# Kernel tuning notes

Measured on AMD Instinct MI355X. Metric: run time of the kernel, lower is better.

## Reference

```python
import jax, jax.numpy as jnp
import numpy as np

D = 256      # input_dim
H = 8        # n_heads
HD = D // H  # head_dim = 32
B = 8
S = 127      # seq_len (feature tokens)
N = S + 1    # new_seq (CLS + features)
LN_EPS = 1e-5


def setup_inputs() -> dict:
    key = jax.random.key(0)
    ks = jax.random.split(key, 20)
    g = 0.02
    inp = {
        "desc_embeddings": jax.random.normal(ks[0], (B, S, D), jnp.float32),
        "name_value_embeddings": jax.random.normal(ks[1], (B, N, D), jnp.float32),
        # q/k/v projections (stored [in, out])
        "wq": jax.random.normal(ks[2], (D, D), jnp.float32) * g,
        "bq": jnp.zeros((D,), jnp.float32),
        "wk": jax.random.normal(ks[3], (D, D), jnp.float32) * g,
        "bk": jnp.zeros((D,), jnp.float32),
        "wv": jax.random.normal(ks[4], (D, D), jnp.float32) * g,
        "bv": jnp.zeros((D,), jnp.float32),
        # edge_update: Linear(2D->D), LayerNorm(D), ReLU, Linear(D->D)
        "ew1": jax.random.normal(ks[5], (2 * D, D), jnp.float32) * g,
        "eb1": jnp.zeros((D,), jnp.float32),
        "ln_g": jnp.ones((D,), jnp.float32),
        "ln_b": jnp.zeros((D,), jnp.float32),
        "ew2": jax.random.normal(ks[6], (D, D), jnp.float32) * g,
        "eb2": jnp.zeros((D,), jnp.float32),
        # attn_proj: Linear(3*head_dim -> 1)
        "attn_w": jax.random.normal(ks[7], (3 * HD,), jnp.float32) * g,
        "attn_b": jnp.zeros((), jnp.float32),
        # out_proj
        "wo": jax.random.normal(ks[8], (D, D), jnp.float32) * g,
        "bo": jnp.zeros((D,), jnp.float32),
    }
    return inp


def _forward(desc, nv, wq, bq, wk, bk, wv, bv, ew1, eb1, ln_g, ln_b, ew2, eb2,
             attn_w, attn_b, wo, bo):
    b, n, d = nv.shape
    s = n - 1
    # new adjacency: [1:,1:] = ones minus diag; row 0 (CLS->var) = 1; col 0 = 0; [0,0]=0
    adj = jnp.zeros((n, n), nv.dtype)
    adj = adj.at[1:, 1:].set(1.0 - jnp.eye(s, dtype=nv.dtype))
    adj = adj.at[0, 1:].set(1.0)
    adj = jnp.broadcast_to(adj, (b, n, n))  # [B,N,N]

    # edge attributes: var-var pairs concat(desc_i, desc_j); CLS row/col concat(desc_j, desc_j)
    var_edge = jnp.concatenate([
        jnp.broadcast_to(desc[:, :, None, :], (b, s, s, d)),
        jnp.broadcast_to(desc[:, None, :, :], (b, s, s, d)),
    ], axis=-1)                                   # [B,S,S,2D]
    cls_edge = jnp.concatenate([desc, desc], -1)  # [B,S,2D]
    ea = jnp.zeros((b, n, n, 2 * d), nv.dtype)
    ea = ea.at[:, 1:, 1:, :].set(var_edge)
    ea = ea.at[:, 0, 1:, :].set(cls_edge)
    ea = ea.at[:, 1:, 0, :].set(cls_edge)

    # edge MLP: Linear -> LayerNorm -> ReLU -> Linear
    h = ea @ ew1 + eb1                            # [B,N,N,D]
    mu = jnp.mean(h, -1, keepdims=True)
    var = jnp.mean((h - mu) ** 2, -1, keepdims=True)
    h = (h - mu) * jax.lax.rsqrt(var + LN_EPS) * ln_g + ln_b
    h = jax.nn.relu(h)
    e = h @ ew2 + eb2                             # [B,N,N,D]
    e = e.reshape(b, n, n, H, HD).transpose(0, 3, 1, 2, 4)  # [B,H,N,N,hd]
    e = e * adj[:, None, :, :, None]

    def heads(x, w, bias):
        return (x @ w + bias).reshape(b, n, H, HD).transpose(0, 2, 1, 3)  # [B,H,N,hd]

    q = heads(nv, wq, bq)
    k = heads(nv, wk, bk)
    v = heads(nv, wv, bv)

    # attn_proj(cat(q_i, k_j, e_ij)) decomposes additively over the three chunks
    w_q, w_k, w_e = attn_w[:HD], attn_w[HD:2 * HD], attn_w[2 * HD:]
    aq = jnp.einsum('bhid,d->bhi', q, w_q)
    ak = jnp.einsum('bhjd,d->bhj', k, w_k)
    ae = jnp.einsum('bhijd,d->bhij', e, w_e)
    scores = aq[:, :, :, None] + ak[:, :, None, :] + ae + attn_b  # [B,H,N,N]
    scores = scores + (adj[:, None] == 0).astype(scores.dtype) * (-1e9)
    attn = jax.nn.softmax(scores, axis=-1)

    ctx = jnp.einsum('bhij,bhjd->bhid', attn, v)                  # [B,H,N,hd]
    ctx = ctx.transpose(0, 2, 1, 3).reshape(b, n, d)
    out = ctx @ wo + bo
    return out, attn


def reference(desc_embeddings, name_value_embeddings, wq, bq, wk, bk, wv, bv,
              ew1, eb1, ln_g, ln_b, ew2, eb2, attn_w, attn_b, wo, bo):
    return _forward(desc_embeddings, name_value_embeddings, wq, bq, wk, bk, wv, bv,
                    ew1, eb1, ln_g, ln_b, ew2, eb2, attn_w, attn_b, wo, bo)
```

## Files before the change

kernel.cpp:

```cpp
#include <hip/hip_runtime.h>
#include <math.h>

namespace {
constexpr int D = 256;
constexpr int H = 8;
constexpr int HD = 32;
constexpr int B = 8;
constexpr int S = 127;
constexpr int N = 128;
constexpr float LN_EPS = 1e-5f;

constexpr int WS_P1T = 0;
constexpr int WS_P2T = WS_P1T + B * D * N;
constexpr int WS_V   = WS_P2T + B * D * N;
constexpr int WS_AQ  = WS_V + B * N * D;
constexpr int WS_AK  = WS_AQ + B * H * N;
constexpr int WS_FQK = WS_AK + B * H * N;
constexpr int WS_V2  = WS_FQK + D * 16;
constexpr int WS_BF  = WS_V2 + D * H;
constexpr int WS_ST  = WS_BF + 32;
constexpr int WS_RSTD = WS_ST + B * 512;
constexpr int WS_MB   = WS_RSTD + B * N * N;

typedef float f32x2 __attribute__((ext_vector_type(2)));
union F4 { float4 v; f32x2 h[2]; float f[4]; };
}

__global__ __launch_bounds__(256) void k1_fold(
    const float* __restrict__ wq, const float* __restrict__ wk,
    const float* __restrict__ ew2, const float* __restrict__ bq,
    const float* __restrict__ bk, const float* __restrict__ eb2,
    const float* __restrict__ attn_w, float* __restrict__ ws) {
  float* FQK = ws + WS_FQK;
  float* V2T = ws + WS_V2;
  float* BF  = ws + WS_BF;
  const int tg = blockIdx.x * 256 + threadIdx.x;
  if (tg < 6144) {
    const int mat = tg >> 11;
    const int rem = tg & 2047;
    const int c = rem >> 3;
    const int h = rem & 7;
    const float* W = (mat == 0) ? wq : (mat == 1) ? wk : ew2;
    const float* aw = attn_w + mat * HD;
    const float* wrow = W + c * D + h * HD;
    float s = 0.f;
#pragma unroll
    for (int d = 0; d < HD; ++d) s = fmaf(wrow[d], aw[d], s);
    if (mat < 2) FQK[c * 16 + mat * 8 + h] = s;
    else         V2T[h * D + c] = s;
  } else if (tg < 6168) {
    const int idx = tg - 6144;
    const int mat = idx >> 3;
    const int h = idx & 7;
    const float* bias = (mat == 0) ? bq : (mat == 1) ? bk : eb2;
    const float* aw = attn_w + mat * HD;
    float s = 0.f;
#pragma unroll
    for (int d = 0; d < HD; ++d) s = fmaf(bias[h * HD + d], aw[d], s);
    BF[mat * 8 + h] = s;
  }
}

__global__ __launch_bounds__(256) void kA_pre(
    const float* __restrict__ desc, const float* __restrict__ ew1,
    const float* __restrict__ eb1,
    const float* __restrict__ nv, const float* __restrict__ wv,
    const float* __restrict__ bv, float* __restrict__ ws) {
  const int blk = blockIdx.x;
  const int t = threadIdx.x;
  __shared__ float rows[4][264];
  __shared__ float aqred[4][64];
  __shared__ float statred[4][16];

  if (blk < 256) {
    float* P1Tf = ws + WS_P1T;
    float* P2Tf = ws + WS_P2T;
    const int b = blk >> 5;
    const int i0 = (blk & 31) * 4;
    for (int k = t; k < 4 * D; k += 256) {
      const int r = k >> 8, c = k & (D - 1);
      const int row = i0 + r;
      rows[r][c] = (row < S) ? desc[(b * S + row) * D + c] : 0.f;
    }
    __syncthreads();
    float a1[4], a2[4];
#pragma unroll
    for (int ii = 0; ii < 4; ++ii) { a1[ii] = 0.f; a2[ii] = 0.f; }
    for (int c2 = 0; c2 < D; c2 += 4) {
      float w1[4], w2[4];
#pragma unroll
      for (int e = 0; e < 4; ++e) {
        w1[e] = ew1[(c2 + e) * D + t];
        w2[e] = ew1[(D + c2 + e) * D + t];
      }
#pragma unroll
      for (int ii = 0; ii < 4; ++ii) {
        F4 dv; dv.v = *(const float4*)&rows[ii][c2];
#pragma unroll
        for (int e = 0; e < 4; ++e) {
          a1[ii] = fmaf(dv.f[e], w1[e], a1[ii]);
          a2[ii] = fmaf(dv.f[e], w2[e], a2[ii]);
        }
      }
    }
    const float ebv = eb1[t];
    const int pbase = (b * 64 + (t >> 2)) * 512 + (t & 3);
#pragma unroll
    for (int ii = 0; ii < 4; ++ii) {
      if (i0 + ii < S) {
        P1Tf[pbase + (i0 + ii) * 4] = a1[ii] + ebv;
        P2Tf[pbase + (i0 + ii) * 4] = a2[ii];
      }
    }
    float stv[16];
#pragma unroll
    for (int ii = 0; ii < 4; ++ii) {
      const float v1 = a1[ii] + ebv;
      const float v2x = a2[ii];
      stv[ii * 4 + 0] = v1;
      stv[ii * 4 + 1] = v1 * v1;
      stv[ii * 4 + 2] = v2x;
      stv[ii * 4 + 3] = v2x * v2x;
    }
#pragma unroll
    for (int st = 0; st < 16; ++st) {
#pragma unroll
      for (int o = 1; o < 64; o <<= 1) stv[st] += __shfl_xor(stv[st], o);
    }
    const int w = t >> 6;
    if ((t & 63) == 0) {
#pragma unroll
      for (int st = 0; st < 16; ++st) statred[w][st] = stv[st];
    }
    __syncthreads();
    if (t < 16) {
      const int ii = t >> 2, st = t & 3;
      if (i0 + ii < S) {
        const float s = statred[0][t] + statred[1][t]
                      + statred[2][t] + statred[3][t];
        ws[WS_ST + b * 512 + st * 128 + (i0 + ii)] = s;
      }
    }
  } else {
    float* Vf  = ws + WS_V;
    float* AQ  = ws + WS_AQ;
    float* AK  = ws + WS_AK;
    const float* FQK = ws + WS_FQK;
    const float* BF  = ws + WS_BF;
    const int blk2 = blk - 256;
    const int b = blk2 >> 5;
    const int j0 = (blk2 & 31) * 4;
    for (int k = t; k < 4 * D; k += 256) {
      const int r = k >> 8, c = k & (D - 1);
      rows[r][c] = nv[(b * N + j0 + r) * D + c];
    }
    __syncthreads();
    float acc[4];
#pragma unroll
    for (int jj = 0; jj < 4; ++jj) acc[jj] = 0.f;
    for (int c2 = 0; c2 < D; c2 += 4) {
      float wvv[4];
#pragma unroll
      for (int e = 0; e < 4; ++e) wvv[e] = wv[(c2 + e) * D + t];
#pragma unroll
      for (int jj = 0; jj < 4; ++jj) {
        F4 x; x.v = *(const float4*)&rows[jj][c2];
#pragma unroll
        for (int e = 0; e < 4; ++e) acc[jj] = fmaf(x.f[e], wvv[e], acc[jj]);
      }
    }
    const float bias = bv[t];
#pragma unroll
    for (int jj = 0; jj < 4; ++jj)
      Vf[(b * N + j0 + jj) * D + t] = acc[jj] + bias;

    const int pair = t & 63;
    const int cq = t >> 6;
    const int il = pair >> 4, oi = pair & 15;
    float s = 0.f;
    for (int c = cq * 64; c < cq * 64 + 64; ++c)
      s = fmaf(rows[il][c], FQK[c * 16 + oi], s);
    aqred[cq][pair] = s;
    __syncthreads();
    if (t < 64) {
      const int il2 = t >> 4, oi2 = t & 15;
      float s2 = aqred[0][t] + aqred[1][t] + aqred[2][t] + aqred[3][t] + BF[oi2];
      if (oi2 < 8) AQ[(b * H + oi2) * N + j0 + il2] = s2;
      else         AK[(b * H + (oi2 - 8)) * N + j0 + il2] = s2;
    }
  }
}

__global__ __launch_bounds__(512) void kG_stats(float* __restrict__ ws) {
  const int bid = blockIdx.x;
  const int wg = (bid & 7) * 32 + (bid >> 3);
  const int b = wg >> 5;
  const int ip0 = (wg & 31) * 4;
  const int t = threadIdx.x;
  const int jp = t & 127;
  const int cg = t >> 7;

  __shared__ float p1t[1024];
  __shared__ float gred[4][4][128];

  const float* P1Tf = ws + WS_P1T;
  const float4* P24 = reinterpret_cast<const float4*>(ws + WS_P2T);
  const float* ST = ws + WS_ST + b * 512;
  float* RST = ws + WS_RSTD + b * N * N;
  float* MBP = ws + WS_MB + b * N * N;
  const int base4 = b * 64 * 128;

  for (int k = t; k < 1024; k += 512) {
    const int r = k >> 8, c = k & 255;
    const int row = ip0 + r;
    p1t[r * 256 + c] = (row < S)
        ? P1Tf[(b * 64 + (c >> 2)) * 512 + row * 4 + (c & 3)] : 0.f;
  }
  F4 pp[16];
#pragma unroll
  for (int cc = 0; cc < 16; ++cc)
    pp[cc].v = P24[base4 + (cg * 16 + cc) * 128 + jp];
  __syncthreads();

  float g[4] = {0.f, 0.f, 0.f, 0.f};
#pragma unroll
  for (int cc = 0; cc < 16; ++cc) {
    const int c4 = cg * 16 + cc;
#pragma unroll
    for (int r = 0; r < 4; ++r) {
      F4 p1; p1.v = *(const float4*)&p1t[r * 256 + c4 * 4];
      g[r] = fmaf(pp[cc].f[0], p1.f[0], g[r]);
      g[r] = fmaf(pp[cc].f[1], p1.f[1], g[r]);
      g[r] = fmaf(pp[cc].f[2], p1.f[2], g[r]);
      g[r] = fmaf(pp[cc].f[3], p1.f[3], g[r]);
    }
  }
#pragma unroll
  for (int r = 0; r < 4; ++r) gred[cg][r][jp] = g[r];
  __syncthreads();
  {
    const int r2 = t >> 7, jp2 = t & 127;
    const float G = gred[0][r2][jp2] + gred[1][r2][jp2]
                  + gred[2][r2][jp2] + gred[3][r2][jp2];
    const int ip = ip0 + r2;
    const float S1 = ST[0 * 128 + ip], Q1 = ST[1 * 128 + ip];
    const float S2 = ST[2 * 128 + jp2], Q2 = ST[3 * 128 + jp2];
    const float mean = (S1 + S2) * (1.f / 256.f);
    const float var = (Q1 + Q2 + 2.f * G) * (1.f / 256.f) - mean * mean;
    const float rstd = 1.f / sqrtf(var + LN_EPS);
    RST[ip * N + jp2] = rstd;
    MBP[ip * N + jp2] = -mean * rstd;
  }
}

__global__ __launch_bounds__(512) void k4_attn(
    const float* __restrict__ ws,
    const float* __restrict__ ln_g, const float* __restrict__ ln_b,
    const float* __restrict__ attn_bp, float* __restrict__ attnp) {
  const int bid = blockIdx.x;
  const int wg = (bid & 7) * 64 + (bid >> 3);
  const int b = wg >> 6;
  const int i0 = (wg & 63) * 2;
  const int t = threadIdx.x;
  const int jl = t & 127;
  const int cq = t >> 7;

  __shared__ float v2s[H * D];
  __shared__ float gbs[2 * D];
  __shared__ float p1e[2][D];
  __shared__ float dsh[4][128][9];
  __shared__ float aqs[2][8];
  __shared__ float redm[8][2], reds[8][2];

  const float* P1Tf = ws + WS_P1T;
  const float* AQ   = ws + WS_AQ;
  const float* AK   = ws + WS_AK;
  const float* BF   = ws + WS_BF;
  const float* v2p  = ws + WS_V2;
  const float* RST  = ws + WS_RSTD + b * N * N;
  const float* MBP  = ws + WS_MB + b * N * N;

  reinterpret_cast<float4*>(v2s)[t] = reinterpret_cast<const float4*>(v2p)[t];
  if (t < 256) { gbs[t] = ln_g[t]; gbs[256 + t] = ln_b[t]; }
  {
    const int r = t >> 8, c = t & 255;
    const int row = i0 + r - 1;
    p1e[r][c] = (row >= 0)
        ? P1Tf[(b * 64 + (c >> 2)) * 512 + row * 4 + (c & 3)] : 0.f;
  }
  if (t < 16) {
    const int r = t >> 3, h = t & 7;
    aqs[r][h] = AQ[(b * H + h) * N + i0 + r] + BF[16 + h] + attn_bp[0];
  }

  const int jm1 = (jl == 0) ? 0 : jl - 1;
  const bool blk0 = (i0 == 0);
  f32x2 rstd2[2], mb2[2];
#pragma unroll
  for (int r = 0; r < 2; ++r) {
    const int irow = i0 + r;
    const int ip = (irow == 0) ? jm1 : (irow - 1);
    const float rs = RST[ip * N + jm1];
    const float mb = MBP[ip * N + jm1];
    rstd2[r].x = rs; rstd2[r].y = rs;
    mb2[r].x = mb; mb2[r].y = mb;
  }
  float akr[2];
#pragma unroll
  for (int hh = 0; hh < 2; ++hh)
    akr[hh] = AK[(b * H + cq * 2 + hh) * N + jl];
  const f32x2 zero2 = {0.f, 0.f};
  __syncthreads();

  const float4* P14 = reinterpret_cast<const float4*>(ws + WS_P1T);
  const float4* P24 = reinterpret_cast<const float4*>(ws + WS_P2T);
  const int base4 = b * 64 * 128;
  const int c4lo = cq * 16;

  f32x2 dt2[2][8];
#pragma unroll
  for (int r = 0; r < 2; ++r)
#pragma unroll
    for (int h = 0; h < 8; ++h) dt2[r][h] = zero2;
  F4 p2c;
  p2c.v = P24[base4 + c4lo * 128 + jm1];
  for (int cc = 0; cc < 16; ++cc) {
    const int c4 = c4lo + cc;
    F4 p2 = p2c;
    if (cc < 15) p2c.v = P24[base4 + (c4 + 1) * 128 + jm1];
    F4 g4; g4.v = *(const float4*)&gbs[c4 * 4];
    F4 b4; b4.v = *(const float4*)&gbs[256 + c4 * 4];
    F4 p1r[2];
    if (blk0) p1r[0].v = P14[base4 + c4 * 128 + jm1];
    else      p1r[0].v = *(const float4*)&p1e[0][c4 * 4];
    p1r[1].v = *(const float4*)&p1e[1][c4 * 4];
    f32x2 w2[2][2];
#pragma unroll
    for (int r = 0; r < 2; ++r) {
#pragma unroll
      for (int pp = 0; pp < 2; ++pp) {
        const f32x2 u2 = p1r[r].h[pp] + p2.h[pp];
        const f32x2 zt2 = __builtin_elementwise_fma(u2, rstd2[r], mb2[r]);
        const f32x2 z2 = __builtin_elementwise_fma(zt2, g4.h[pp], b4.h[pp]);
        w2[r][pp] = __builtin_elementwise_max(z2, zero2);
      }
    }
#pragma unroll
    for (int h = 0; h < 8; ++h) {
      F4 v2v; v2v.v = *(const float4*)&v2s[h * D + c4 * 4];
      dt2[0][h] = __builtin_elementwise_fma(w2[0][0], v2v.h[0], dt2[0][h]);
      dt2[0][h] = __builtin_elementwise_fma(w2[0][1], v2v.h[1], dt2[0][h]);
      dt2[1][h] = __builtin_elementwise_fma(w2[1][0], v2v.h[0], dt2[1][h]);
      dt2[1][h] = __builtin_elementwise_fma(w2[1][1], v2v.h[1], dt2[1][h]);
    }
  }

  const int w = t >> 6;
  for (int r = 0; r < 2; ++r) {
#pragma unroll
    for (int h = 0; h < 8; ++h) dsh[cq][jl][h] = dt2[r][h].x + dt2[r][h].y;
    __syncthreads();
    const int irow = i0 + r;
    const bool masked = (jl == 0) || (jl == irow);
    float sc[2], pr[2];
#pragma unroll
    for (int hh = 0; hh < 2; ++hh) {
      const int h = cq * 2 + hh;
      const float dsum = dsh[0][jl][h] + dsh[1][jl][h]
                       + dsh[2][jl][h] + dsh[3][jl][h];
      const float v = aqs[r][h] + akr[hh] + dsum;
      sc[hh] = masked ? -INFINITY : v;
    }
    float mx[2];
#pragma unroll
    for (int hh = 0; hh < 2; ++hh) {
      float v = sc[hh];
#pragma unroll
      for (int o = 1; o < 64; o <<= 1) v = fmaxf(v, __shfl_xor(v, o));
      mx[hh] = v;
    }
    if ((t & 63) == 0) { redm[w][0] = mx[0]; redm[w][1] = mx[1]; }
    __syncthreads();
#pragma unroll
    for (int hh = 0; hh < 2; ++hh) {
      const float m = fmaxf(redm[w][hh], redm[w ^ 1][hh]);
      pr[hh] = expf(sc[hh] - m);
    }
    float sm[2];
#pragma unroll
    for (int hh = 0; hh < 2; ++hh) {
      float v = pr[hh];
#pragma unroll
      for (int o = 1; o < 64; o <<= 1) v += __shfl_xor(v, o);
      sm[hh] = v;
    }
    if ((t & 63) == 0) { reds[w][0] = sm[0]; reds[w][1] = sm[1]; }
    __syncthreads();
#pragma unroll
    for (int hh = 0; hh < 2; ++hh) {
      const int h = cq * 2 + hh;
      const float at = pr[hh] / (reds[w][hh] + reds[w ^ 1][hh]);
      attnp[((b * H + h) * N + irow) * N + jl] = at;
    }
    __syncthreads();
  }
}

__global__ __launch_bounds__(1024) void k5_out(
    const float* __restrict__ ws, const float* __restrict__ attnp,
    const float* __restrict__ wo, const float* __restrict__ bo,
    float* __restrict__ outp) {
  const int bid = blockIdx.x;
  const int wg = (bid & 7) * 32 + (bid >> 3);
  const int b = wg >> 5;
  const int i0 = (wg & 31) * 4;
  const int t = threadIdx.x;
  const int r = t >> 8, c = t & 255;

  __shared__ float attn_sh[4][H][N];
  __shared__ float ctxs[4][260];

  for (int k = t; k < 4 * H * N; k += 1024) {
    const int rr = k >> 10, h = (k >> 7) & 7, j = k & 127;
    attn_sh[rr][h][j] = attnp[((b * H + h) * N + i0 + rr) * N + j];
  }
  __syncthreads();

  const int hh = c >> 5;
  const float* Vb = ws + WS_V + b * N * D + c;
  float acc = 0.f;
  for (int j = 0; j < N; ++j)
    acc = fmaf(attn_sh[r][hh][j], Vb[j * D], acc);
  ctxs[r][c] = acc;
  __syncthreads();

  float o = bo[c];
  for (int c2 = 0; c2 < D; c2 += 4) {
    F4 cx; cx.v = *(const float4*)&ctxs[r][c2];
    o = fmaf(cx.f[0], wo[(c2 + 0) * D + c], o);
    o = fmaf(cx.f[1], wo[(c2 + 1) * D + c], o);
    o = fmaf(cx.f[2], wo[(c2 + 2) * D + c], o);
    o = fmaf(cx.f[3], wo[(c2 + 3) * D + c], o);
  }
  outp[(b * N + i0 + r) * D + c] = o;
}

extern "C" void kernel_launch(void* const* d_in, const int* in_sizes, int n_in,
                              void* d_out, int out_size, void* d_ws, size_t ws_size,
                              hipStream_t stream) {
  (void)in_sizes; (void)n_in; (void)out_size; (void)ws_size;
  const float* desc = (const float*)d_in[0];
  const float* nv   = (const float*)d_in[1];
  const float* wq   = (const float*)d_in[2];
  const float* bq   = (const float*)d_in[3];
  const float* wk   = (const float*)d_in[4];
  const float* bk   = (const float*)d_in[5];
  const float* wv   = (const float*)d_in[6];
  const float* bv   = (const float*)d_in[7];
  const float* ew1  = (const float*)d_in[8];
  const float* eb1  = (const float*)d_in[9];
  const float* ln_g = (const float*)d_in[10];
  const float* ln_b = (const float*)d_in[11];
  const float* ew2  = (const float*)d_in[12];
  const float* eb2  = (const float*)d_in[13];
  const float* aw   = (const float*)d_in[14];
  const float* ab   = (const float*)d_in[15];
  const float* wo   = (const float*)d_in[16];
  const float* bo   = (const float*)d_in[17];

  float* ws   = (float*)d_ws;
  float* outp = (float*)d_out;
  float* attnp = outp + B * N * D;

  k1_fold<<<25, 256, 0, stream>>>(wq, wk, ew2, bq, bk, eb2, aw, ws);
  kA_pre<<<512, 256, 0, stream>>>(desc, ew1, eb1, nv, wv, bv, ws);
  kG_stats<<<256, 512, 0, stream>>>(ws);
  k4_attn<<<B * 64, 512, 0, stream>>>(ws, ln_g, ln_b, ab, attnp);
  k5_out<<<256, 1024, 0, stream>>>(ws, attnp, wo, bo, outp);
}
```

Measured before the change: 56.75 us.

## Restructure pre and output kernels with float4 register tiling and split-K reductions

The P1/P2 projection, the V projection and the output kernel now use float4 weight loads with per-thread register tiles over output columns and rows. The output kernel drops from 1024 to 512 threads and splits the j and K dimensions across thread groups, adding a shared-memory reduction step. The FQK matrix is staged in shared memory for the aq/ak dot products, and the per-row stats reduction is simplified. This is meant to cut redundant scalar global weight loads and improve memory coalescing. The cost is extra shared memory, more synchronization, and an idle-thread imbalance in the V path, where only 64 threads do the GEMM.

```diff
diff --git a/kernel.cpp b/kernel.cpp
--- a/kernel.cpp
+++ b/kernel.cpp
@@ -69,77 +69,73 @@
   const int blk = blockIdx.x;
   const int t = threadIdx.x;
   __shared__ float rows[4][264];
-  __shared__ float aqred[4][64];
-  __shared__ float statred[4][16];
+  __shared__ float fqks[D * 16];
+  __shared__ float aqred2[2][64];
 
   if (blk < 256) {
     float* P1Tf = ws + WS_P1T;
     float* P2Tf = ws + WS_P2T;
     const int b = blk >> 5;
     const int i0 = (blk & 31) * 4;
-    for (int k = t; k < 4 * D; k += 256) {
-      const int r = k >> 8, c = k & (D - 1);
+    {
+      const int r = t >> 6, c4 = t & 63;
       const int row = i0 + r;
-      rows[r][c] = (row < S) ? desc[(b * S + row) * D + c] : 0.f;
-    }
-    __syncthreads();
-    float a1[4], a2[4];
-#pragma unroll
-    for (int ii = 0; ii < 4; ++ii) { a1[ii] = 0.f; a2[ii] = 0.f; }
-    for (int c2 = 0; c2 < D; c2 += 4) {
-      float w1[4], w2[4];
+      F4 dv;
+      if (row < S) dv.v = *(const float4*)&desc[(b * S + row) * D + c4 * 4];
+      else         dv.v = make_float4(0.f, 0.f, 0.f, 0.f);
+      *(float4*)&rows[r][c4 * 4] = dv.v;
+    }
+    __syncthreads();
+    const int o4 = t & 63;
+    const int grp = t >> 6;
+    const int m = grp >> 1;
+    const int rp = grp & 1;
+    const float* W = ew1 + m * D * D;
+    F4 a0, a1;
+    a0.v = make_float4(0.f, 0.f, 0.f, 0.f);
+    a1.v = make_float4(0.f, 0.f, 0.f, 0.f);
+    for (int c2 = 0; c2 < D; ++c2) {
+      F4 w; w.v = *(const float4*)&W[c2 * D + o4 * 4];
+      const float s0 = rows[rp * 2][c2];
+      const float s1 = rows[rp * 2 + 1][c2];
 #pragma unroll
       for (int e = 0; e < 4; ++e) {
-        w1[e] = ew1[(c2 + e) * D + t];
-        w2[e] = ew1[(D + c2 + e) * D + t];
+        a0.f[e] = fmaf(s0, w.f[e], a0.f[e]);
+        a1.f[e] = fmaf(s1, w.f[e], a1.f[e]);
       }
-#pragma unroll
-      for (int ii = 0; ii < 4; ++ii) {
-        F4 dv; dv.v = *(const float4*)&rows[ii][c2];
-#pragma unroll
-        for (int e = 0; e < 4; ++e) {
-          a1[ii] = fmaf(dv.f[e], w1[e], a1[ii]);
-          a2[ii] = fmaf(dv.f[e], w2[e], a2[ii]);
-        }
-      }
-    }
-    const float ebv = eb1[t];
-    const int pbase = (b * 64 + (t >> 2)) * 512 + (t & 3);
-#pragma unroll
-    for (int ii = 0; ii < 4; ++ii) {
-      if (i0 + ii < S) {
-        P1Tf[pbase + (i0 + ii) * 4] = a1[ii] + ebv;
-        P2Tf[pbase + (i0 + ii) * 4] = a2[ii];
-      }
-    }
-    float stv[16];
-#pragma unroll
-    for (int ii = 0; ii < 4; ++ii) {
-      const float v1 = a1[ii] + ebv;
-      const float v2x = a2[ii];
-      stv[ii * 4 + 0] = v1;
-      stv[ii * 4 + 1] = v1 * v1;
-      stv[ii * 4 + 2] = v2x;
-      stv[ii * 4 + 3] = v2x * v2x;
-    }
-#pragma unroll
-    for (int st = 0; st < 16; ++st) {
-#pragma unroll
-      for (int o = 1; o < 64; o <<= 1) stv[st] += __shfl_xor(stv[st], o);
-    }
-    const int w = t >> 6;
-    if ((t & 63) == 0) {
-#pragma unroll
-      for (int st = 0; st < 16; ++st) statred[w][st] = stv[st];
-    }
-    __syncthreads();
-    if (t < 16) {
-      const int ii = t >> 2, st = t & 3;
-      if (i0 + ii < S) {
-        const float s = statred[0][t] + statred[1][t]
-                      + statred[2][t] + statred[3][t];
-        ws[WS_ST + b * 512 + st * 128 + (i0 + ii)] = s;
-      }
+    }
+    F4 ebv;
+    if (m == 0) ebv.v = *(const float4*)&eb1[o4 * 4];
+    else        ebv.v = make_float4(0.f, 0.f, 0.f, 0.f);
+    F4 o0, o1;
+#pragma unroll
+    for (int e = 0; e < 4; ++e) {
+      o0.f[e] = a0.f[e] + ebv.f[e];
+      o1.f[e] = a1.f[e] + ebv.f[e];
+    }
+    float* PT = (m == 0) ? P1Tf : P2Tf;
+    const int rbase = (b * 64 + o4) * 512;
+    const int row0i = i0 + rp * 2;
+    const int row1i = row0i + 1;
+    if (row0i < S) *(float4*)&PT[rbase + row0i * 4] = o0.v;
+    if (row1i < S) *(float4*)&PT[rbase + row1i * 4] = o1.v;
+    float sv0 = 0.f, qv0 = 0.f, sv1 = 0.f, qv1 = 0.f;
+#pragma unroll
+    for (int e = 0; e < 4; ++e) {
+      sv0 += o0.f[e]; qv0 = fmaf(o0.f[e], o0.f[e], qv0);
+      sv1 += o1.f[e]; qv1 = fmaf(o1.f[e], o1.f[e], qv1);
+    }
+#pragma unroll
+    for (int o = 1; o < 64; o <<= 1) {
+      sv0 += __shfl_xor(sv0, o);
+      qv0 += __shfl_xor(qv0, o);
+      sv1 += __shfl_xor(sv1, o);
+      qv1 += __shfl_xor(qv1, o);
+    }
+    if (o4 == 0) {
+      float* STW = ws + WS_ST + b * 512 + m * 256;
+      if (row0i < S) { STW[row0i] = sv0; STW[128 + row0i] = qv0; }
+      if (row1i < S) { STW[row1i] = sv1; STW[128 + row1i] = qv1; }
     }
   } else {
     float* Vf  = ws + WS_V;
@@ -150,43 +146,54 @@
     const int blk2 = blk - 256;
     const int b = blk2 >> 5;
     const int j0 = (blk2 & 31) * 4;
-    for (int k = t; k < 4 * D; k += 256) {
-      const int r = k >> 8, c = k & (D - 1);
-      rows[r][c] = nv[(b * N + j0 + r) * D + c];
-    }
-    __syncthreads();
-    float acc[4];
-#pragma unroll
-    for (int jj = 0; jj < 4; ++jj) acc[jj] = 0.f;
-    for (int c2 = 0; c2 < D; c2 += 4) {
-      float wvv[4];
-#pragma unroll
-      for (int e = 0; e < 4; ++e) wvv[e] = wv[(c2 + e) * D + t];
-#pragma unroll
-      for (int jj = 0; jj < 4; ++jj) {
-        F4 x; x.v = *(const float4*)&rows[jj][c2];
-#pragma unroll
-        for (int e = 0; e < 4; ++e) acc[jj] = fmaf(x.f[e], wvv[e], acc[jj]);
+    {
+      const int r = t >> 6, c4 = t & 63;
+      *(float4*)&rows[r][c4 * 4] =
+          *(const float4*)&nv[(b * N + j0 + r) * D + c4 * 4];
+      float4* fq4 = (float4*)fqks;
+      const float4* FQK4 = (const float4*)FQK;
+#pragma unroll
+      for (int k = 0; k < 4; ++k) fq4[k * 256 + t] = FQK4[k * 256 + t];
+    }
+    __syncthreads();
+    if (t < 64) {
+      const int o4 = t;
+      F4 acc[4];
+#pragma unroll
+      for (int r = 0; r < 4; ++r) acc[r].v = make_float4(0.f, 0.f, 0.f, 0.f);
+      for (int c2 = 0; c2 < D; ++c2) {
+        F4 w; w.v = *(const float4*)&wv[c2 * D + o4 * 4];
+#pragma unroll
+        for (int r = 0; r < 4; ++r) {
+          const float s = rows[r][c2];
+#pragma unroll
+          for (int e = 0; e < 4; ++e)
+            acc[r].f[e] = fmaf(s, w.f[e], acc[r].f[e]);
+        }
       }
-    }
-    const float bias = bv[t];
-#pragma unroll
-    for (int jj = 0; jj < 4; ++jj)
-      Vf[(b * N + j0 + jj) * D + t] = acc[jj] + bias;
-
-    const int pair = t & 63;
-    const int cq = t >> 6;
-    const int il = pair >> 4, oi = pair & 15;
-    float s = 0.f;
-    for (int c = cq * 64; c < cq * 64 + 64; ++c)
-      s = fmaf(rows[il][c], FQK[c * 16 + oi], s);
-    aqred[cq][pair] = s;
+      F4 b4; b4.v = *(const float4*)&bv[o4 * 4];
+#pragma unroll
+      for (int r = 0; r < 4; ++r) {
+#pragma unroll
+        for (int e = 0; e < 4; ++e) acc[r].f[e] += b4.f[e];
+        *(float4*)&Vf[(b * N + j0 + r) * D + o4 * 4] = acc[r].v;
+      }
+    } else if (t < 192) {
+      const int idx = t - 64;
+      const int il = idx >> 5;
+      const int oi = idx & 15;
+      const int ch = (idx >> 4) & 1;
+      float s = 0.f;
+      for (int c = ch * 128; c < ch * 128 + 128; ++c)
+        s = fmaf(rows[il][c], fqks[c * 16 + oi], s);
+      aqred2[ch][il * 16 + oi] = s;
+    }
     __syncthreads();
     if (t < 64) {
-      const int il2 = t >> 4, oi2 = t & 15;
-      float s2 = aqred[0][t] + aqred[1][t] + aqred[2][t] + aqred[3][t] + BF[oi2];
-      if (oi2 < 8) AQ[(b * H + oi2) * N + j0 + il2] = s2;
-      else         AK[(b * H + (oi2 - 8)) * N + j0 + il2] = s2;
+      const int il = t >> 4, oi = t & 15;
+      const float s2 = aqred2[0][t] + aqred2[1][t] + BF[oi];
+      if (oi < 8) AQ[(b * H + oi) * N + j0 + il] = s2;
+      else        AK[(b * H + (oi - 8)) * N + j0 + il] = s2;
     }
   }
 }
@@ -406,7 +413,7 @@
   }
 }
 
-__global__ __launch_bounds__(1024) void k5_out(
+__global__ __launch_bounds__(512) void k5_out(
     const float* __restrict__ ws, const float* __restrict__ attnp,
     const float* __restrict__ wo, const float* __restrict__ bo,
     float* __restrict__ outp) {
@@ -415,34 +422,82 @@
   const int b = wg >> 5;
   const int i0 = (wg & 31) * 4;
   const int t = threadIdx.x;
-  const int r = t >> 8, c = t & 255;
-
-  __shared__ float attn_sh[4][H][N];
+  const int o4 = t & 63;
+  const int grp = t >> 6;
+
+  __shared__ float attn_sh[4][H][136];
+  __shared__ float red[4][8][64][4];
   __shared__ float ctxs[4][260];
 
-  for (int k = t; k < 4 * H * N; k += 1024) {
-    const int rr = k >> 10, h = (k >> 7) & 7, j = k & 127;
-    attn_sh[rr][h][j] = attnp[((b * H + h) * N + i0 + rr) * N + j];
-  }
-  __syncthreads();
-
-  const int hh = c >> 5;
-  const float* Vb = ws + WS_V + b * N * D + c;
-  float acc = 0.f;
-  for (int j = 0; j < N; ++j)
-    acc = fmaf(attn_sh[r][hh][j], Vb[j * D], acc);
-  ctxs[r][c] = acc;
-  __syncthreads();
-
-  float o = bo[c];
-  for (int c2 = 0; c2 < D; c2 += 4) {
-    F4 cx; cx.v = *(const float4*)&ctxs[r][c2];
-    o = fmaf(cx.f[0], wo[(c2 + 0) * D + c], o);
-    o = fmaf(cx.f[1], wo[(c2 + 1) * D + c], o);
-    o = fmaf(cx.f[2], wo[(c2 + 2) * D + c], o);
-    o = fmaf(cx.f[3], wo[(c2 + 3) * D + c], o);
-  }
-  outp[(b * N + i0 + r) * D + c] = o;
+#pragma unroll
+  for (int k = 0; k < 2; ++k) {
+    const int idx = k * 512 + t;
+    const int r = idx >> 8, h = (idx >> 5) & 7, j4 = idx & 31;
+    const float4 a =
+        *(const float4*)&attnp[((b * H + h) * N + i0 + r) * N + j4 * 4];
+    *(float4*)&attn_sh[r][h][j4 * 4] = a;
+  }
+  __syncthreads();
+
+  const int hh = o4 >> 3;
+  const float* Vb = ws + WS_V + b * N * D;
+  F4 acc[4];
+#pragma unroll
+  for (int r = 0; r < 4; ++r) acc[r].v = make_float4(0.f, 0.f, 0.f, 0.f);
+  for (int jj = 0; jj < 16; ++jj) {
+    const int j = grp * 16 + jj;
+    F4 v4; v4.v = *(const float4*)&Vb[j * D + o4 * 4];
+#pragma unroll
+    for (int r = 0; r < 4; ++r) {
+      const float a = attn_sh[r][hh][j];
+#pragma unroll
+      for (int e = 0; e < 4; ++e) acc[r].f[e] = fmaf(a, v4.f[e], acc[r].f[e]);
+    }
+  }
+#pragma unroll
+  for (int r = 0; r < 4; ++r) *(float4*)&red[r][grp][o4][0] = acc[r].v;
+  __syncthreads();
+  if (t < 256) {
+    const int oc = t & 63, r = t >> 6;
+    F4 s; s.v = make_float4(0.f, 0.f, 0.f, 0.f);
+#pragma unroll
+    for (int g = 0; g < 8; ++g) {
+      F4 p; p.v = *(const float4*)&red[r][g][oc][0];
+#pragma unroll
+      for (int e = 0; e < 4; ++e) s.f[e] += p.f[e];
+    }
+    *(float4*)&ctxs[r][oc * 4] = s.v;
+  }
+  __syncthreads();
+
+  F4 acc2[4];
+#pragma unroll
+  for (int r = 0; r < 4; ++r) acc2[r].v = make_float4(0.f, 0.f, 0.f, 0.f);
+  for (int cc = 0; cc < 32; ++cc) {
+    const int c2 = grp * 32 + cc;
+    F4 w4; w4.v = *(const float4*)&wo[c2 * D + o4 * 4];
+#pragma unroll
+    for (int r = 0; r < 4; ++r) {
+      const float cx = ctxs[r][c2];
+#pragma unroll
+      for (int e = 0; e < 4; ++e)
+        acc2[r].f[e] = fmaf(cx, w4.f[e], acc2[r].f[e]);
+    }
+  }
+#pragma unroll
+  for (int r = 0; r < 4; ++r) *(float4*)&red[r][grp][o4][0] = acc2[r].v;
+  __syncthreads();
+  if (t < 256) {
+    const int oc = t & 63, r = t >> 6;
+    F4 s; s.v = *(const float4*)&bo[oc * 4];
+#pragma unroll
+    for (int g = 0; g < 8; ++g) {
+      F4 p; p.v = *(const float4*)&red[r][g][oc][0];
+#pragma unroll
+      for (int e = 0; e < 4; ++e) s.f[e] += p.f[e];
+    }
+    *(float4*)&outp[(b * N + i0 + r) * D + oc * 4] = s.v;
+  }
 }
 
 extern "C" void kernel_launch(void* const* d_in, const int* in_sizes, int n_in,
@@ -476,5 +531,5 @@
   kA_pre<<<512, 256, 0, stream>>>(desc, ew1, eb1, nv, wv, bv, ws);
   kG_stats<<<256, 512, 0, stream>>>(ws);
   k4_attn<<<B * 64, 512, 0, stream>>>(ws, ln_g, ln_b, ab, attnp);
-  k5_out<<<256, 1024, 0, stream>>>(ws, attnp, wo, bo, outp);
-}
+  k5_out<<<256, 512, 0, stream>>>(ws, attnp, wo, bo, outp);
+}
```

After: 52.61 us. -7.3%, faster.
